# Performance work log

Hardware: AMD Instinct MI355X
Metric: run time of the kernel (lower is better)

## Reference

```python
import jax, jax.numpy as jnp
import numpy as np

GAMMA = 0.01


def softor(x, axis, gamma=GAMMA):
    # gamma * logsumexp(x/gamma) with NSFR-style normalization when max > 1
    ls = gamma * jax.nn.logsumexp(x / gamma, axis=axis)
    return ls / jnp.maximum(jnp.max(ls), 1.0)


def clause_eval(x, I, gamma=GAMMA):
    # x: [B, G] valuations; I: [C, G, S, L] int indices into G
    gathered = x[:, I]                      # [B, C, G, S, L]  (gather along G)
    body = jnp.prod(gathered, axis=-1)      # [B, C, G, S]  product over body atoms
    return softor(body, axis=-1, gamma=gamma)  # [B, C, G]  soft-OR over substitutions


def r_step(x, W, I, gamma=GAMMA):
    C = clause_eval(x, I, gamma)            # [B, C, G]
    W_star = jax.nn.softmax(W, axis=1)      # [m, C]
    H = jnp.einsum('mc,bcg->mbg', W_star, C)  # [m, B, G]
    return softor(H, axis=0, gamma=gamma)   # [B, G]


def reference(x, W, I, infer_step):
    R = x
    for _ in range(infer_step):
        R = softor(jnp.stack([R, r_step(R, W, I)], axis=1), axis=1)  # [B, G]
    return R


def setup_inputs():
    key = jax.random.key(0)
    k1, k2, k3 = jax.random.split(key, 3)
    B, G, C, S, L, m = 16, 8192, 16, 8, 3, 1
    x = jax.random.uniform(k1, (B, G), dtype=jnp.float32)
    I = jax.random.randint(k2, (C, G, S, L), 0, G, dtype=jnp.int32)
    W = jax.random.uniform(k3, (m, C), dtype=jnp.float32)
    return {"x": x, "W": W, "I": I, "infer_step": 4}
```

## Files before the change

kernel.cpp:

```cpp
#include <hip/hip_runtime.h>
#include <hip/hip_fp16.h>

constexpr int B = 16;
constexpr int G = 8192;
constexpr int C = 16;
constexpr int S = 8;
constexpr int L = 3;
constexpr int STEPS = 4;
constexpr int NSLOT = 64;
constexpr int ARR = NSLOT * 16;

#define K_E   144.269504088896f
#define GLN2  0.00693147180560f

typedef float f4 __attribute__((ext_vector_type(4)));

__device__ __forceinline__ float fexp2(float x){ return __builtin_amdgcn_exp2f(x); }
__device__ __forceinline__ float flog2(float x){ return __builtin_amdgcn_logf(x); }

__device__ __forceinline__ void atomicMaxF(float* p, float v){
    atomicMax(reinterpret_cast<unsigned int*>(p), __float_as_uint(v));
}

__device__ __forceinline__ float waveMax(float v){
    #pragma unroll
    for (int off = 32; off > 0; off >>= 1)
        v = fmaxf(v, __shfl_down(v, off));
    return v;
}

__device__ __forceinline__ float waveSlotMax(const float* __restrict__ slots){
    float v = slots[(threadIdx.x & 63) << 4];
    v = fmaxf(v, __shfl_xor(v, 32));
    v = fmaxf(v, __shfl_xor(v, 16));
    v = fmaxf(v, __shfl_xor(v, 8));
    v = fmaxf(v, __shfl_xor(v, 4));
    v = fmaxf(v, __shfl_xor(v, 2));
    v = fmaxf(v, __shfl_xor(v, 1));
    return __builtin_amdgcn_readfirstlane(v);
}

template<bool PK>
__global__ __launch_bounds__(256) void prep_kernel(
        const float* __restrict__ x, const int* __restrict__ I,
        const float* __restrict__ W,
        float* __restrict__ wstar, float* __restrict__ slots,
        ushort* __restrict__ Ipk,
        float* __restrict__ T0, __half* __restrict__ Thh0)
{
    constexpr int NPACK = PK ? (C*G*S*L/4)/256 : 0;
    const int bid = blockIdx.x;
    if (PK && bid < NPACK){
        int t = bid*256 + threadIdx.x;
        int4 v = ((const int4*)I)[t];
        ushort4 o;
        o.x = (ushort)v.x; o.y = (ushort)v.y; o.z = (ushort)v.z; o.w = (ushort)v.w;
        ((ushort4*)Ipk)[t] = o;
    } else if (bid < NPACK + (B*G)/256){
        int t = (bid - NPACK)*256 + threadIdx.x;
        int b = t >> 13;
        int g = t & (G-1);
        float v = x[t];
        T0[g*B + b] = v;
        if (PK) Thh0[((size_t)(b>>3)*G + g)*8 + (b&7)] = __float2half(v);
    } else {
        int t = threadIdx.x;
        for (int i = t; i < 13*ARR; i += 256) slots[i] = 0.f;
        if (t == 0){
            slots[12*ARR] = 1.0f;
            float mx = -1e30f;
            for (int c = 0; c < C; c++) mx = fmaxf(mx, W[c]);
            float e[C]; float s = 0.f;
            for (int c = 0; c < C; c++){ e[c] = fexp2((W[c]-mx)*1.44269504089f); s += e[c]; }
            for (int c = 0; c < C; c++) wstar[c] = e[c] / s;
        }
    }
}

__global__ __launch_bounds__(1024) void clause_lds(
        const __half*  __restrict__ Thh,
        const ushort*  __restrict__ I16,
        const float*   __restrict__ wstar,
        const float*   __restrict__ slotPrev,
        float* __restrict__ slotLs,
        float* __restrict__ slotHu,
        float* __restrict__ Hu)
{
    extern __shared__ __align__(16) uint4 sSt4[];

    const int tix = threadIdx.x;
    const int bh  = blockIdx.x >> 7;
    const int g0  = (blockIdx.x & 127) * 64;

    const uint4* src = (const uint4*)(Thh + (size_t)bh*G*8);
    #pragma unroll
    for (int r = 0; r < 8; r++) sSt4[tix + r*1024] = src[tix + r*1024];

    const float scPrev = 1.0f / fmaxf(waveSlotMax(slotPrev), 1.0f);
    const float sc3 = scPrev * scPrev * scPrev;

    __syncthreads();

    const int lane = tix & 63;
    const int wib  = tix >> 6;
    const int c    = lane & 15;
    const int gsub = lane >> 4;
    const int g    = g0 + wib*4 + gsub;
    const float wc = wstar[c];

    const uint4* ip = (const uint4*)(I16 + ((size_t)c*G + g)*24);
    uint4 q0 = ip[0], q1 = ip[1], q2 = ip[2];
    unsigned dw[12] = {q0.x,q0.y,q0.z,q0.w, q1.x,q1.y,q1.z,q1.w,
                       q2.x,q2.y,q2.z,q2.w};
    int ix[24];
    #pragma unroll
    for (int i = 0; i < 12; i++){
        ix[2*i]   = (int)(dw[i] & 0xFFFFu);
        ix[2*i+1] = (int)(dw[i] >> 16);
    }

    float body[S][8];
    #pragma unroll
    for (int s = 0; s < S; s++){
        uint4 r0 = sSt4[ix[3*s+0]];
        uint4 r1 = sSt4[ix[3*s+1]];
        uint4 r2 = sSt4[ix[3*s+2]];
        #pragma unroll
        for (int h = 0; h < 4; h++){
            float2 a  = __half22float2(((const __half2*)&r0)[h]);
            float2 b2 = __half22float2(((const __half2*)&r1)[h]);
            float2 c2 = __half22float2(((const __half2*)&r2)[h]);
            body[s][2*h]   = a.x*b2.x*c2.x*sc3;
            body[s][2*h+1] = a.y*b2.y*c2.y*sc3;
        }
    }

    float hu[8];
    float lsm = 0.f;
    #pragma unroll
    for (int bl = 0; bl < 8; bl++){
        float m = body[0][bl];
        #pragma unroll
        for (int s = 1; s < S; s++) m = fmaxf(m, body[s][bl]);
        float sum = 0.f;
        #pragma unroll
        for (int s = 0; s < S; s++) sum += fexp2((body[s][bl] - m) * K_E);
        float ls = m + GLN2 * flog2(sum);
        lsm = fmaxf(lsm, ls);
        hu[bl] = wc * ls;
    }

    #pragma unroll
    for (int bl = 0; bl < 8; bl++){
        hu[bl] += __shfl_xor(hu[bl], 1);
        hu[bl] += __shfl_xor(hu[bl], 2);
        hu[bl] += __shfl_xor(hu[bl], 4);
        hu[bl] += __shfl_xor(hu[bl], 8);
    }
    float humax = hu[0];
    #pragma unroll
    for (int bl = 1; bl < 8; bl++) humax = fmaxf(humax, hu[bl]);

    if (c == 0){
        f4 v0 = {hu[0], hu[1], hu[2], hu[3]};
        f4 v1 = {hu[4], hu[5], hu[6], hu[7]};
        *(f4*)(Hu + (size_t)g*B + bh*8)     = v0;
        *(f4*)(Hu + (size_t)g*B + bh*8 + 4) = v1;
    }

    float wl = waveMax(lsm);
    float wh = waveMax(humax);
    if (lane == 0){
        const int wv = blockIdx.x*16 + wib;
        atomicMaxF(&slotLs[(wv & (NSLOT-1)) << 4], wl);
        atomicMaxF(&slotHu[(wv & (NSLOT-1)) << 4], wh);
    }
}

__global__ __launch_bounds__(256) void clause_bh(
        const __half*  __restrict__ Thh,
        const ushort*  __restrict__ I16,
        const float*   __restrict__ wstar,
        const float*   __restrict__ slotPrev,
        float* __restrict__ slotLs,
        float* __restrict__ slotHu,
        float* __restrict__ Hu)
{
    const int lane = threadIdx.x & 63;
    const int g    = blockIdx.x*4 + (threadIdx.x >> 6);
    const int j    = lane >> 4;
    const int b    = lane & 15;
    const __half* Tb = Thh + (size_t)(b>>3)*G*8 + (b&7);

    const float scPrev = 1.0f / fmaxf(waveSlotMax(slotPrev), 1.0f);
    const float sc3 = scPrev * scPrev * scPrev;
    const f4 wst4 = *(const f4*)(wstar + j*4);

    float humix = 0.f, lsmax = 0.f;
    #pragma unroll 2
    for (int k = 0; k < 4; k++){
        const int c = j*4 + k;
        const uint4* p = (const uint4*)(I16 + (size_t)(c*G + g)*(S*L));
        uint4 d0 = p[0], d1 = p[1], d2 = p[2];
        unsigned dw[12] = {d0.x,d0.y,d0.z,d0.w, d1.x,d1.y,d1.z,d1.w,
                           d2.x,d2.y,d2.z,d2.w};
        float gv[S*L];
        #pragma unroll
        for (int i = 0; i < 12; i++){
            gv[2*i]   = __half2float(Tb[(size_t)(dw[i] & 0xFFFFu)*8]);
            gv[2*i+1] = __half2float(Tb[(size_t)(dw[i] >> 16)*8]);
        }
        float body[S];
        #pragma unroll
        for (int s = 0; s < S; s++) body[s] = gv[3*s]*gv[3*s+1]*gv[3*s+2]*sc3;

        float m = body[0];
        #pragma unroll
        for (int s = 1; s < S; s++) m = fmaxf(m, body[s]);
        float sum = 0.f;
        #pragma unroll
        for (int s = 0; s < S; s++) sum += fexp2((body[s] - m) * K_E);
        float ls = m + GLN2 * flog2(sum);

        lsmax = fmaxf(lsmax, ls);
        humix = __builtin_fmaf(wst4[k], ls, humix);
    }
    humix += __shfl_xor(humix, 16);
    humix += __shfl_xor(humix, 32);
    if (lane < 16) Hu[(size_t)g*B + lane] = humix;

    float wl = waveMax(lsmax);
    float wh = waveMax(humix);
    if (lane == 0){
        atomicMaxF(&slotLs[(g & (NSLOT-1)) << 4], wl);
        atomicMaxF(&slotHu[(g & (NSLOT-1)) << 4], wh);
    }
}

__global__ __launch_bounds__(256) void clause_f(
        const float* __restrict__ Tin,
        const int*   __restrict__ I32,
        const float* __restrict__ wstar,
        const float* __restrict__ slotPrev,
        float* __restrict__ slotLs,
        float* __restrict__ slotHu,
        float* __restrict__ Hu)
{
    const int lane = threadIdx.x & 63;
    const int g    = blockIdx.x*4 + (threadIdx.x >> 6);
    const int j    = lane >> 4;
    const int b    = lane & 15;

    const float scPrev = 1.0f / fmaxf(waveSlotMax(slotPrev), 1.0f);
    const float sc3 = scPrev * scPrev * scPrev;
    const f4 wst4 = *(const f4*)(wstar + j*4);

    float humix = 0.f, lsmax = 0.f;
    #pragma unroll 2
    for (int k = 0; k < 4; k++){
        const int c = j*4 + k;
        const int4* p = (const int4*)(I32 + (size_t)(c*G + g)*(S*L));
        int idx[S*L];
        #pragma unroll
        for (int i = 0; i < 6; i++){
            int4 v = p[i];
            idx[4*i] = v.x; idx[4*i+1] = v.y; idx[4*i+2] = v.z; idx[4*i+3] = v.w;
        }
        float gv[S*L];
        #pragma unroll
        for (int t = 0; t < S*L; t++) gv[t] = Tin[idx[t]*B + b];

        float body[S];
        #pragma unroll
        for (int s = 0; s < S; s++) body[s] = gv[3*s]*gv[3*s+1]*gv[3*s+2]*sc3;

        float m = body[0];
        #pragma unroll
        for (int s = 1; s < S; s++) m = fmaxf(m, body[s]);
        float sum = 0.f;
        #pragma unroll
        for (int s = 0; s < S; s++) sum += fexp2((body[s] - m) * K_E);
        float ls = m + GLN2 * flog2(sum);

        lsmax = fmaxf(lsmax, ls);
        humix = __builtin_fmaf(wst4[k], ls, humix);
    }
    humix += __shfl_xor(humix, 16);
    humix += __shfl_xor(humix, 32);
    if (lane < 16) Hu[(size_t)g*B + lane] = humix;

    float wl = waveMax(lsmax);
    float wh = waveMax(humix);
    if (lane == 0){
        atomicMaxF(&slotLs[(g & (NSLOT-1)) << 4], wl);
        atomicMaxF(&slotHu[(g & (NSLOT-1)) << 4], wh);
    }
}

template<bool PK>
__global__ __launch_bounds__(256) void combine_kernel(
        const float* __restrict__ Hu,
        const float* __restrict__ Tin,
        const float* __restrict__ slotLs,
        const float* __restrict__ slotHu,
        const float* __restrict__ slotPrev,
        float* __restrict__ Tout,
        __half* __restrict__ Touth,
        float* __restrict__ slotT)
{
    const float scA = 1.0f / fmaxf(waveSlotMax(slotLs), 1.0f);
    const float scB = 1.0f / fmaxf(scA * waveSlotMax(slotHu), 1.0f);
    const float scP = 1.0f / fmaxf(waveSlotMax(slotPrev), 1.0f);

    const int t = blockIdx.x*256 + threadIdx.x;
    float r  = Hu[t] * (scA * scB);
    float Rn = Tin[t] * scP;
    float M  = fmaxf(Rn, r);
    float v  = M + GLN2 * flog2(fexp2((Rn-M)*K_E) + fexp2((r-M)*K_E));
    Tout[t] = v;
    if (PK){
        int g = t >> 4, b = t & 15;
        Touth[((size_t)(b>>3)*G + g)*8 + (b&7)] = __float2half(v);
    }
    float wm = waveMax(v);
    if ((threadIdx.x & 63) == 0)
        atomicMaxF(&slotT[(blockIdx.x & (NSLOT-1)) << 4], wm);
}

__global__ void output_kernel(const float* __restrict__ T, const float* __restrict__ slotT,
                              float* __restrict__ out){
    float sc = 1.0f / fmaxf(waveSlotMax(slotT), 1.0f);
    int tid = blockIdx.x*256 + threadIdx.x;
    int b = tid >> 13;
    int g = tid & (G-1);
    out[tid] = T[g*B + b] * sc;
}

extern "C" void kernel_launch(void* const* d_in, const int* in_sizes, int n_in,
                              void* d_out, int out_size, void* d_ws, size_t ws_size,
                              hipStream_t stream) {
    const float* x = (const float*)d_in[0];
    const float* W = (const float*)d_in[1];
    const int*   I = (const int*)d_in[2];

    const size_t baseF  = 16 + 13*ARR;
    const size_t packF  = (size_t)C*G*S*L / 2;
    const size_t stateF = (size_t)G*B;
    const size_t halfF  = (size_t)G*B / 2;
    const bool packed = ws_size >= (baseF + packF + 3*stateF + 2*halfF) * sizeof(float);

    float* ws    = (float*)d_ws;
    float* wstar = ws;
    float* slots = ws + 16;
    ushort* Ipk  = (ushort*)(ws + baseF);
    float* T0    = ws + baseF + (packed ? packF : 0);
    float* T1    = T0 + stateF;
    float* Hu    = T1 + stateF;
    __half* Thh0 = (__half*)(Hu + stateF);
    __half* Thh1 = Thh0 + (size_t)G*B;

    float* out = (float*)d_out;

    bool ldsOK = false;
    if (packed)
        ldsOK = hipFuncSetAttribute((const void*)clause_lds,
                    hipFuncAttributeMaxDynamicSharedMemorySize, 131072) == hipSuccess;

    if (packed){
        prep_kernel<true><<<(C*G*S*L/4)/256 + (B*G)/256 + 1, 256, 0, stream>>>(
            x, I, W, wstar, slots, Ipk, T0, Thh0);
    } else {
        prep_kernel<false><<<(B*G)/256 + 1, 256, 0, stream>>>(
            x, I, W, wstar, slots, Ipk, T0, Thh0);
    }

    float*  bufs[2]  = {T0, T1};
    __half* bufsh[2] = {Thh0, Thh1};
    for (int s = 0; s < STEPS; s++){
        float*  Tin   = bufs[s & 1];
        float*  Tout  = bufs[(s+1) & 1];
        __half* Tinh  = bufsh[s & 1];
        __half* Touth = bufsh[(s+1) & 1];
        float* slotLs = slots + (s*3 + 0)*ARR;
        float* slotHu = slots + (s*3 + 1)*ARR;
        float* slotT  = slots + (s*3 + 2)*ARR;
        const float* slotPrev = (s == 0) ? (slots + 12*ARR) : (slots + ((s-1)*3 + 2)*ARR);
        if (packed){
            if (ldsOK)
                clause_lds<<<256, 1024, 131072, stream>>>(Tinh, Ipk, wstar, slotPrev,
                                                          slotLs, slotHu, Hu);
            else
                clause_bh<<<G/4, 256, 0, stream>>>(Tinh, Ipk, wstar, slotPrev,
                                                   slotLs, slotHu, Hu);
            combine_kernel<true><<<(G*B)/256, 256, 0, stream>>>(Hu, Tin, slotLs, slotHu,
                                                                slotPrev, Tout, Touth, slotT);
        } else {
            clause_f<<<G/4, 256, 0, stream>>>(Tin, I, wstar, slotPrev,
                                              slotLs, slotHu, Hu);
            combine_kernel<false><<<(G*B)/256, 256, 0, stream>>>(Hu, Tin, slotLs, slotHu,
                                                                 slotPrev, Tout, Touth, slotT);
        }
    }
    output_kernel<<<(B*G)/256, 256, 0, stream>>>(bufs[STEPS & 1],
                                                 slots + ((STEPS-1)*3 + 2)*ARR, out);
}
```

Before: 71.93 us.

## Fuse all inference steps into one persistent kernel with tree grid barriers

Replaces the multi-kernel sequence (prep, per-step clause/combine kernels, output) with one persistent kernel of 256 blocks of 1024 threads. Grid-wide phases are separated by a hierarchical atomic barrier in global memory. Each step reloads the half-precision state into LDS, evaluates the clauses, and then applies the normalization and soft-OR combine in place. The aim is to remove kernel launch gaps and per-launch overhead. The cost is spin-wait barriers that depend on all 256 blocks being co-resident, which deadlocks otherwise, plus an extra memset launch.

```diff
diff --git a/kernel.cpp b/kernel.cpp
--- a/kernel.cpp
+++ b/kernel.cpp
@@ -9,6 +9,8 @@
 constexpr int STEPS = 4;
 constexpr int NSLOT = 64;
 constexpr int ARR = NSLOT * 16;
+constexpr int NBLK = 256;
+constexpr int TPB  = 1024;
 
 #define K_E   144.269504088896f
 #define GLN2  0.00693147180560f
@@ -38,6 +40,202 @@
     v = fmaxf(v, __shfl_xor(v, 2));
     v = fmaxf(v, __shfl_xor(v, 1));
     return __builtin_amdgcn_readfirstlane(v);
+}
+
+__device__ __forceinline__ void treeBar(unsigned* bar, int ep){
+    __syncthreads();
+    if (threadIdx.x == 0){
+        unsigned* grp = bar + ((blockIdx.x & 7) << 4);
+        unsigned r = __hip_atomic_fetch_add(grp, 1u, __ATOMIC_ACQ_REL,
+                                            __HIP_MEMORY_SCOPE_AGENT);
+        if (r + 1u == (unsigned)(ep*32)){
+            unsigned q = __hip_atomic_fetch_add(bar + 128, 1u, __ATOMIC_ACQ_REL,
+                                                __HIP_MEMORY_SCOPE_AGENT);
+            if (q + 1u == (unsigned)(ep*8))
+                __hip_atomic_store(bar + 144, (unsigned)ep, __ATOMIC_RELEASE,
+                                   __HIP_MEMORY_SCOPE_AGENT);
+        }
+        while (__hip_atomic_load(bar + 144, __ATOMIC_ACQUIRE,
+                                 __HIP_MEMORY_SCOPE_AGENT) < (unsigned)ep)
+            __builtin_amdgcn_s_sleep(4);
+    }
+    __syncthreads();
+}
+
+__global__ void __launch_bounds__(TPB) fused_kernel(
+        const float* __restrict__ x, const int* __restrict__ I,
+        const float* __restrict__ W,
+        float* __restrict__ slots, unsigned* __restrict__ bar,
+        ushort* __restrict__ Ipk,
+        float* __restrict__ T,
+        __half* __restrict__ Thh,
+        float* __restrict__ Hu,
+        float* __restrict__ out)
+{
+    extern __shared__ __align__(16) uint4 sSt4[];
+    __shared__ float sW[16];
+    __shared__ float sWm[8];
+
+    const int tix = threadIdx.x;
+    const int bid = blockIdx.x;
+    const int gt  = bid*TPB + tix;
+    const int bh  = bid >> 7;
+    const int g0  = (bid & 127) * 64;
+
+    {
+        const int4* I4 = (const int4*)I;
+        ushort4* P4 = (ushort4*)Ipk;
+        #pragma unroll
+        for (int k = 0; k < 3; k++){
+            int i = gt + k*(NBLK*TPB);
+            int4 v = I4[i];
+            ushort4 o;
+            o.x = (ushort)v.x; o.y = (ushort)v.y; o.z = (ushort)v.z; o.w = (ushort)v.w;
+            P4[i] = o;
+        }
+    }
+    if (gt < B*G){
+        int b = gt >> 13, g = gt & (G-1);
+        float v = x[gt];
+        T[g*B + b] = v;
+        Thh[((size_t)(b>>3)*G + g)*8 + (b&7)] = __float2half(v);
+    }
+    if (gt < 12*ARR) slots[gt] = 0.f;
+    if (tix < 16){
+        float w = W[tix];
+        float m = w;
+        #pragma unroll
+        for (int o = 8; o; o >>= 1) m = fmaxf(m, __shfl_xor(m, o));
+        float e = fexp2((w - m)*1.44269504089f);
+        float ssum = e;
+        #pragma unroll
+        for (int o = 8; o; o >>= 1) ssum += __shfl_xor(ssum, o);
+        sW[tix] = e / ssum;
+    }
+
+    int ep = 1;
+    treeBar(bar, ep++);
+
+    float scPrev = 1.0f;
+
+    for (int s = 0; s < STEPS; s++){
+        float* slotLs = slots + (s*3 + 0)*ARR;
+        float* slotHu = slots + (s*3 + 1)*ARR;
+        float* slotT  = slots + (s*3 + 2)*ARR;
+
+        const uint4* src = (const uint4*)(Thh + (size_t)bh*G*8);
+        #pragma unroll
+        for (int r = 0; r < 8; r++) sSt4[tix + r*1024] = src[tix + r*1024];
+        __syncthreads();
+
+        const float sc3 = scPrev*scPrev*scPrev;
+        const int lane = tix & 63;
+        const int wib  = tix >> 6;
+        const int c    = lane & 15;
+        const int gsub = lane >> 4;
+        const int g    = g0 + wib*4 + gsub;
+        const float wc = sW[c];
+
+        const uint4* ip = (const uint4*)(Ipk + ((size_t)c*G + g)*24);
+        uint4 q0 = ip[0], q1 = ip[1], q2 = ip[2];
+        unsigned dw[12] = {q0.x,q0.y,q0.z,q0.w, q1.x,q1.y,q1.z,q1.w,
+                           q2.x,q2.y,q2.z,q2.w};
+        int ix[24];
+        #pragma unroll
+        for (int i = 0; i < 12; i++){
+            ix[2*i]   = (int)(dw[i] & 0xFFFFu);
+            ix[2*i+1] = (int)(dw[i] >> 16);
+        }
+
+        float body[S][8];
+        #pragma unroll
+        for (int ss = 0; ss < S; ss++){
+            uint4 r0 = sSt4[ix[3*ss+0]];
+            uint4 r1 = sSt4[ix[3*ss+1]];
+            uint4 r2 = sSt4[ix[3*ss+2]];
+            #pragma unroll
+            for (int h = 0; h < 4; h++){
+                float2 a  = __half22float2(((const __half2*)&r0)[h]);
+                float2 b2 = __half22float2(((const __half2*)&r1)[h]);
+                float2 c2 = __half22float2(((const __half2*)&r2)[h]);
+                body[ss][2*h]   = a.x*b2.x*c2.x*sc3;
+                body[ss][2*h+1] = a.y*b2.y*c2.y*sc3;
+            }
+        }
+
+        float hu[8];
+        float lsm = 0.f;
+        #pragma unroll
+        for (int bl = 0; bl < 8; bl++){
+            float m = body[0][bl];
+            #pragma unroll
+            for (int ss = 1; ss < S; ss++) m = fmaxf(m, body[ss][bl]);
+            float sum = 0.f;
+            #pragma unroll
+            for (int ss = 0; ss < S; ss++) sum += fexp2((body[ss][bl] - m) * K_E);
+            float ls = m + GLN2 * flog2(sum);
+            lsm = fmaxf(lsm, ls);
+            hu[bl] = wc * ls;
+        }
+        #pragma unroll
+        for (int bl = 0; bl < 8; bl++){
+            hu[bl] += __shfl_xor(hu[bl], 1);
+            hu[bl] += __shfl_xor(hu[bl], 2);
+            hu[bl] += __shfl_xor(hu[bl], 4);
+            hu[bl] += __shfl_xor(hu[bl], 8);
+        }
+        float humax = hu[0];
+        #pragma unroll
+        for (int bl = 1; bl < 8; bl++) humax = fmaxf(humax, hu[bl]);
+
+        if (c == 0){
+            f4 v0 = {hu[0], hu[1], hu[2], hu[3]};
+            f4 v1 = {hu[4], hu[5], hu[6], hu[7]};
+            *(f4*)(Hu + (size_t)g*B + bh*8)     = v0;
+            *(f4*)(Hu + (size_t)g*B + bh*8 + 4) = v1;
+        }
+        float wl = waveMax(lsm);
+        float wh = waveMax(humax);
+        if (lane == 0){
+            const int wv = bid*16 + wib;
+            atomicMaxF(&slotLs[(wv & (NSLOT-1)) << 4], wl);
+            atomicMaxF(&slotHu[(wv & (NSLOT-1)) << 4], wh);
+        }
+
+        treeBar(bar, ep++);
+
+        const float scA = 1.0f / fmaxf(waveSlotMax(slotLs), 1.0f);
+        const float scB = 1.0f / fmaxf(scA * waveSlotMax(slotHu), 1.0f);
+        float v = 0.f;
+        int gc = 0, bc = 0;
+        if (tix < 512){
+            gc = bid*32 + (tix >> 4);
+            bc = tix & 15;
+            float r  = Hu[gc*B + bc] * (scA * scB);
+            float Rn = T[gc*B + bc] * scPrev;
+            float M  = fmaxf(Rn, r);
+            v = M + GLN2 * flog2(fexp2((Rn-M)*K_E) + fexp2((r-M)*K_E));
+            if (s < STEPS-1){
+                T[gc*B + bc] = v;
+                Thh[((size_t)(bc>>3)*G + gc)*8 + (bc&7)] = __float2half(v);
+            }
+        }
+        float wm = waveMax(v);
+        if ((tix & 63) == 0 && tix < 512) sWm[tix >> 6] = wm;
+        __syncthreads();
+        if (tix == 0){
+            float bm = sWm[0];
+            #pragma unroll
+            for (int i2 = 1; i2 < 8; i2++) bm = fmaxf(bm, sWm[i2]);
+            atomicMaxF(&slotT[(bid & (NSLOT-1)) << 4], bm);
+        }
+
+        treeBar(bar, ep++);
+
+        scPrev = 1.0f / fmaxf(waveSlotMax(slotT), 1.0f);
+        if (s == STEPS-1 && tix < 512)
+            out[bc*G + gc] = v * scPrev;
+    }
 }
 
 template<bool PK>
@@ -149,7 +347,6 @@
         lsm = fmaxf(lsm, ls);
         hu[bl] = wc * ls;
     }
-
     #pragma unroll
     for (int bl = 0; bl < 8; bl++){
         hu[bl] += __shfl_xor(hu[bl], 1);
@@ -343,13 +540,37 @@
     const float* W = (const float*)d_in[1];
     const int*   I = (const int*)d_in[2];
 
-    const size_t baseF  = 16 + 13*ARR;
+    float* ws  = (float*)d_ws;
+    float* out = (float*)d_out;
+
     const size_t packF  = (size_t)C*G*S*L / 2;
     const size_t stateF = (size_t)G*B;
+    const size_t fSlots = 0;
+    const size_t fBar   = 12*ARR;
+    const size_t fIpk   = fBar + 160;
+    const size_t fT     = fIpk + packF;
+    const size_t fThh   = fT + stateF;
+    const size_t fHu    = fThh + stateF/2;
+    const size_t fTotal = fHu + stateF;
+
+    bool fusedOK = ws_size >= fTotal * sizeof(float);
+    if (fusedOK)
+        fusedOK = hipFuncSetAttribute((const void*)fused_kernel,
+                      hipFuncAttributeMaxDynamicSharedMemorySize, 131072) == hipSuccess;
+
+    if (fusedOK){
+        unsigned* bar = (unsigned*)(ws + fBar);
+        hipMemsetAsync(bar, 0, 1024, stream);
+        fused_kernel<<<NBLK, TPB, 131072, stream>>>(
+            x, I, W, ws + fSlots, bar, (ushort*)(ws + fIpk),
+            ws + fT, (__half*)(ws + fThh), ws + fHu, out);
+        return;
+    }
+
+    const size_t baseF  = 16 + 13*ARR;
     const size_t halfF  = (size_t)G*B / 2;
     const bool packed = ws_size >= (baseF + packF + 3*stateF + 2*halfF) * sizeof(float);
 
-    float* ws    = (float*)d_ws;
     float* wstar = ws;
     float* slots = ws + 16;
     ushort* Ipk  = (ushort*)(ws + baseF);
@@ -358,8 +579,6 @@
     float* Hu    = T1 + stateF;
     __half* Thh0 = (__half*)(Hu + stateF);
     __half* Thh1 = Thh0 + (size_t)G*B;
-
-    float* out = (float*)d_out;
 
     bool ldsOK = false;
     if (packed)
```

After: 250.5 us. +248.3%, slower.
